# Kernel optimization log

Hardware: AMD Instinct MI355X
Metric: run time of the kernel (lower is better)

The kernel has to match this reference:

```python
import jax, jax.numpy as jnp
import numpy as np

N, NFEAT, NHID, K = 10000, 3000, 32, 10
ALPHA = 0.2


def setup_inputs() -> dict:
    key = jax.random.key(0)
    k1, k2, k3, k4, k5 = jax.random.split(key, 5)
    stdv = 1.0 / np.sqrt(NHID)
    x = jax.random.normal(k1, (N, NFEAT), dtype=jnp.float32)
    adj = jax.random.uniform(k2, (N, N), dtype=jnp.float32) / N  # row-stochastic-ish
    W = jax.random.uniform(k3, (NFEAT, NHID), minval=-stdv, maxval=stdv, dtype=jnp.float32)
    b = jax.random.uniform(k4, (NHID,), minval=-stdv, maxval=stdv, dtype=jnp.float32)
    mu = jax.random.normal(k5, (K, NHID), dtype=jnp.float32)
    return {"x": x, "adj": adj, "W": W, "b": b, "mu": mu}


def reference(x, adj, W, b, mu):
    # GCN layer: adj @ (x @ W) + b
    support = jnp.matmul(x, W)            # [N, NHID]
    z = jnp.matmul(adj, support) + b      # [N, NHID]
    # Student-t soft assignment (computed without materializing [N, K, NHID]):
    # ||z_i - mu_j||^2 = |z_i|^2 - 2 z_i.mu_j + |mu_j|^2
    z2 = jnp.sum(z * z, axis=1, keepdims=True)        # [N, 1]
    mu2 = jnp.sum(mu * mu, axis=1)                    # [K]
    d2 = z2 - 2.0 * jnp.matmul(z, mu.T) + mu2         # [N, K]
    q = 1.0 / (1.0 + d2 / ALPHA + 1e-08)
    q = q ** (ALPHA + 1.0) / 2.0
    q = q / jnp.sum(q, axis=1, keepdims=True)
    return z, q
```

## Files before the change

kernel.cpp:

```cpp
#include <hip/hip_runtime.h>
#include <math.h>


#define NH     32
#define KC     32
#define TR     256
#define LDA_S  36
#define NSPLIT 16

__global__ __launch_bounds__(256) void gemm_nt32(
    const float* __restrict__ A,
    const float* __restrict__ B,
    float* __restrict__ outp,
    int M, int K, int nchunks)
{
    __shared__ float As[TR * LDA_S];
    __shared__ float Bs[KC * NH];

    const int tid  = threadIdx.x;
    const int rg   = tid >> 2;
    const int jg   = tid & 3;
    const int row0 = blockIdx.x * TR;
    const int sy   = blockIdx.y;

    float acc[4][8];
#pragma unroll
    for (int m = 0; m < 4; ++m)
#pragma unroll
        for (int j = 0; j < 8; ++j) acc[m][j] = 0.0f;

    for (int c = sy; c < nchunks; c += NSPLIT) {
        const int k0 = c * KC;

#pragma unroll
        for (int p = 0; p < 8; ++p) {
            int idx = tid + (p << 8);
            int ar  = idx >> 3;
            int ac4 = idx & 7;
            int gr  = row0 + ar;
            int gk  = k0 + (ac4 << 2);
            float4 v = make_float4(0.f, 0.f, 0.f, 0.f);
            if (gr < M && gk < K)
                v = *(const float4*)(A + (size_t)gr * K + gk);
            *(float4*)(&As[ar * LDA_S + (ac4 << 2)]) = v;
        }
        {
            int brow = tid >> 3;
            int bc4  = tid & 7;
            int gk   = k0 + brow;
            float4 v = make_float4(0.f, 0.f, 0.f, 0.f);
            if (gk < K)
                v = *(const float4*)(B + (size_t)gk * NH + (bc4 << 2));
            *(float4*)(&Bs[brow * NH + (bc4 << 2)]) = v;
        }
        __syncthreads();

#pragma unroll
        for (int kk = 0; kk < KC; kk += 4) {
            float4 a[4];
#pragma unroll
            for (int m = 0; m < 4; ++m)
                a[m] = *(const float4*)(&As[(rg + (m << 6)) * LDA_S + kk]);
#pragma unroll
            for (int t = 0; t < 4; ++t) {
                float4 b0 = *(const float4*)(&Bs[(kk + t) * NH + (jg << 3)]);
                float4 b1 = *(const float4*)(&Bs[(kk + t) * NH + (jg << 3) + 4]);
#pragma unroll
                for (int m = 0; m < 4; ++m) {
                    float av = (t == 0) ? a[m].x : (t == 1) ? a[m].y
                             : (t == 2) ? a[m].z : a[m].w;
                    acc[m][0] += av * b0.x;
                    acc[m][1] += av * b0.y;
                    acc[m][2] += av * b0.z;
                    acc[m][3] += av * b0.w;
                    acc[m][4] += av * b1.x;
                    acc[m][5] += av * b1.y;
                    acc[m][6] += av * b1.z;
                    acc[m][7] += av * b1.w;
                }
            }
        }
        __syncthreads();
    }

    float* op = outp + (size_t)sy * M * NH;
#pragma unroll
    for (int m = 0; m < 4; ++m) {
        int gr = row0 + rg + (m << 6);
        if (gr < M) {
            float4 v0 = make_float4(acc[m][0], acc[m][1], acc[m][2], acc[m][3]);
            float4 v1 = make_float4(acc[m][4], acc[m][5], acc[m][6], acc[m][7]);
            *(float4*)(op + (size_t)gr * NH + (jg << 3))     = v0;
            *(float4*)(op + (size_t)gr * NH + (jg << 3) + 4) = v1;
        }
    }
}

__global__ __launch_bounds__(256) void reduce_add(
    const float* __restrict__ parts,
    const float* __restrict__ bias,
    float* __restrict__ out,
    int total4)
{
    int i = blockIdx.x * blockDim.x + threadIdx.x;
    if (i >= total4) return;
    float4 s = make_float4(0.f, 0.f, 0.f, 0.f);
#pragma unroll
    for (int p = 0; p < NSPLIT; ++p) {
        float4 v = ((const float4*)parts)[(size_t)p * total4 + i];
        s.x += v.x; s.y += v.y; s.z += v.z; s.w += v.w;
    }
    if (bias) {
        float4 bv = ((const float4*)bias)[i & 7];
        s.x += bv.x; s.y += bv.y; s.z += bv.z; s.w += bv.w;
    }
    ((float4*)out)[i] = s;
}

__global__ __launch_bounds__(256) void qkern(
    const float* __restrict__ z,
    const float* __restrict__ mu,
    float* __restrict__ q,
    int N)
{
    const int tid  = threadIdx.x;
    const int lane = tid & 31;
    const int i    = blockIdx.x * 8 + (tid >> 5);
    if (i >= N) return;

    float zv = z[i * 32 + lane];
    float qm = 0.f, qsum = 0.f;
#pragma unroll
    for (int c = 0; c < 10; ++c) {
        float d = zv - mu[c * 32 + lane];
        float p = d * d;
#pragma unroll
        for (int m = 16; m >= 1; m >>= 1) p += __shfl_xor(p, m, 32);
        float t  = 1.0f + p * 5.0f + 1e-8f;
        float qc = powf(t, -1.2f) * 0.5f;
        qsum += qc;
        if (lane == c) qm = qc;
    }
    if (lane < 10) q[i * 10 + lane] = qm / qsum;
}

extern "C" void kernel_launch(void* const* d_in, const int* in_sizes, int n_in,
                              void* d_out, int out_size, void* d_ws, size_t ws_size,
                              hipStream_t stream)
{
    const float* x   = (const float*)d_in[0];
    const float* adj = (const float*)d_in[1];
    const float* W   = (const float*)d_in[2];
    const float* b   = (const float*)d_in[3];
    const float* mu  = (const float*)d_in[4];

    const int N = 10000, NFEAT = 3000;
    float* z_out = (float*)d_out;
    float* q_out = (float*)d_out + N * NH;

    float* ws_part    = (float*)d_ws;
    float* ws_support = (float*)d_ws + (size_t)NSPLIT * N * NH;

    const int total4   = N * NH / 4;
    const int rowBlks  = (N + TR - 1) / TR;
    const int redBlks  = (total4 + 255) / 256;

    {
        int nchunks = (NFEAT + KC - 1) / KC;
        gemm_nt32<<<dim3(rowBlks, NSPLIT), 256, 0, stream>>>(
            x, W, ws_part, N, NFEAT, nchunks);
    }
    reduce_add<<<redBlks, 256, 0, stream>>>(ws_part, nullptr, ws_support, total4);
    {
        int nchunks = (N + KC - 1) / KC;
        gemm_nt32<<<dim3(rowBlks, NSPLIT), 256, 0, stream>>>(
            adj, ws_support, ws_part, N, N, nchunks);
    }
    reduce_add<<<redBlks, 256, 0, stream>>>(ws_part, b, z_out, total4);
    qkern<<<(N + 7) / 8, 256, 0, stream>>>(z_out, mu, q_out, N);
}
```

Measured before the change: 835.5 us.

## Stream A rows directly from global with register double-buffering, contiguous K splits

The skinny GEMM no longer stages the A tile in shared memory. Each thread reads its four rows straight from global memory as float4s, prefetching the next 8-wide chunk into registers while computing the current one. Each block now covers one contiguous K range and loads large 320-row B slabs into LDS, and the split count doubles to 32 when the workspace allows. This removes the LDS round-trip and the per-32-K syncs on the bandwidth-bound adj read, at the cost of uncoalesced per-thread strided global loads and larger partial-sum reductions.

```diff
diff --git a/kernel.cpp b/kernel.cpp
--- a/kernel.cpp
+++ b/kernel.cpp
@@ -2,26 +2,62 @@
 #include <math.h>
 
 
-#define NH     32
-#define KC     32
-#define TR     256
-#define LDA_S  36
-#define NSPLIT 16
-
-__global__ __launch_bounds__(256) void gemm_nt32(
+#define NH   32
+#define SUBK 320
+#define TRB  256
+
+__device__ __forceinline__ void fma8x4(const float4* __restrict__ bs, int jg2,
+                                       const float4* a0, const float4* a1,
+                                       float acc[4][8])
+{
+#pragma unroll
+    for (int u = 0; u < 2; ++u) {
+#pragma unroll
+        for (int t = 0; t < 4; ++t) {
+            float4 b0 = bs[(u * 4 + t) * 8 + jg2];
+            float4 b1 = bs[(u * 4 + t) * 8 + jg2 + 1];
+#pragma unroll
+            for (int m = 0; m < 4; ++m) {
+                float4 am = u ? a1[m] : a0[m];
+                float av = (t == 0) ? am.x : (t == 1) ? am.y
+                         : (t == 2) ? am.z : am.w;
+                acc[m][0] += av * b0.x;
+                acc[m][1] += av * b0.y;
+                acc[m][2] += av * b0.z;
+                acc[m][3] += av * b0.w;
+                acc[m][4] += av * b1.x;
+                acc[m][5] += av * b1.y;
+                acc[m][6] += av * b1.z;
+                acc[m][7] += av * b1.w;
+            }
+        }
+    }
+}
+
+__global__ __launch_bounds__(256) void gemm_stream32(
     const float* __restrict__ A,
     const float* __restrict__ B,
     float* __restrict__ outp,
-    int M, int K, int nchunks)
-{
-    __shared__ float As[TR * LDA_S];
-    __shared__ float Bs[KC * NH];
-
-    const int tid  = threadIdx.x;
-    const int rg   = tid >> 2;
-    const int jg   = tid & 3;
-    const int row0 = blockIdx.x * TR;
-    const int sy   = blockIdx.y;
+    int M, int K, int CH)
+{
+    __shared__ float Bs[SUBK * NH];
+
+    const int tid     = threadIdx.x;
+    const int rowslot = tid >> 2;
+    const int jg      = tid & 3;
+    const int jg2     = jg << 1;
+    const int row0    = blockIdx.x * TRB;
+    const int sy      = blockIdx.y;
+    const int k0      = sy * CH;
+    const int kspl    = min(CH, K - k0);
+
+    const float* ap[4];
+#pragma unroll
+    for (int m = 0; m < 4; ++m) {
+        int r = row0 + rowslot + (m << 6);
+        if (r > M - 1) r = M - 1;
+        ap[m] = A + (size_t)r * K + k0;
+    }
 
     float acc[4][8];
 #pragma unroll
@@ -29,56 +65,42 @@
 #pragma unroll
         for (int j = 0; j < 8; ++j) acc[m][j] = 0.0f;
 
-    for (int c = sy; c < nchunks; c += NSPLIT) {
-        const int k0 = c * KC;
-
-#pragma unroll
-        for (int p = 0; p < 8; ++p) {
-            int idx = tid + (p << 8);
-            int ar  = idx >> 3;
-            int ac4 = idx & 7;
-            int gr  = row0 + ar;
-            int gk  = k0 + (ac4 << 2);
-            float4 v = make_float4(0.f, 0.f, 0.f, 0.f);
-            if (gr < M && gk < K)
-                v = *(const float4*)(A + (size_t)gr * K + gk);
-            *(float4*)(&As[ar * LDA_S + (ac4 << 2)]) = v;
-        }
+    for (int kb = 0; kb < kspl; kb += SUBK) {
+        const int kcnt = min(SUBK, kspl - kb);
+
         {
-            int brow = tid >> 3;
-            int bc4  = tid & 7;
-            int gk   = k0 + brow;
-            float4 v = make_float4(0.f, 0.f, 0.f, 0.f);
-            if (gk < K)
-                v = *(const float4*)(B + (size_t)gk * NH + (bc4 << 2));
-            *(float4*)(&Bs[brow * NH + (bc4 << 2)]) = v;
+            const float4* src = (const float4*)(B + (size_t)(k0 + kb) * NH);
+            float4* dst = (float4*)Bs;
+            for (int i = tid; i < kcnt * 8; i += 256) dst[i] = src[i];
         }
         __syncthreads();
 
-#pragma unroll
-        for (int kk = 0; kk < KC; kk += 4) {
-            float4 a[4];
-#pragma unroll
-            for (int m = 0; m < 4; ++m)
-                a[m] = *(const float4*)(&As[(rg + (m << 6)) * LDA_S + kk]);
-#pragma unroll
-            for (int t = 0; t < 4; ++t) {
-                float4 b0 = *(const float4*)(&Bs[(kk + t) * NH + (jg << 3)]);
-                float4 b1 = *(const float4*)(&Bs[(kk + t) * NH + (jg << 3) + 4]);
+        float4 A0[4], A1[4], B0[4], B1[4];
+#pragma unroll
+        for (int m = 0; m < 4; ++m) {
+            A0[m] = *(const float4*)(ap[m] + kb);
+            A1[m] = *(const float4*)(ap[m] + kb + 4);
+        }
+
+        int kk = 0;
+        for (; kk + 16 <= kcnt; kk += 16) {
+#pragma unroll
+            for (int m = 0; m < 4; ++m) {
+                B0[m] = *(const float4*)(ap[m] + kb + kk + 8);
+                B1[m] = *(const float4*)(ap[m] + kb + kk + 12);
+            }
+            fma8x4(((const float4*)Bs) + kk * 8, jg2, A0, A1, acc);
+            if (kk + 16 < kcnt) {
 #pragma unroll
                 for (int m = 0; m < 4; ++m) {
-                    float av = (t == 0) ? a[m].x : (t == 1) ? a[m].y
-                             : (t == 2) ? a[m].z : a[m].w;
-                    acc[m][0] += av * b0.x;
-                    acc[m][1] += av * b0.y;
-                    acc[m][2] += av * b0.z;
-                    acc[m][3] += av * b0.w;
-                    acc[m][4] += av * b1.x;
-                    acc[m][5] += av * b1.y;
-                    acc[m][6] += av * b1.z;
-                    acc[m][7] += av * b1.w;
+                    A0[m] = *(const float4*)(ap[m] + kb + kk + 16);
+                    A1[m] = *(const float4*)(ap[m] + kb + kk + 20);
                 }
             }
+            fma8x4(((const float4*)Bs) + (kk + 8) * 8, jg2, B0, B1, acc);
+        }
+        if (kk < kcnt) {
+            fma8x4(((const float4*)Bs) + kk * 8, jg2, A0, A1, acc);
         }
         __syncthreads();
     }
@@ -86,7 +108,7 @@
     float* op = outp + (size_t)sy * M * NH;
 #pragma unroll
     for (int m = 0; m < 4; ++m) {
-        int gr = row0 + rg + (m << 6);
+        int gr = row0 + rowslot + (m << 6);
         if (gr < M) {
             float4 v0 = make_float4(acc[m][0], acc[m][1], acc[m][2], acc[m][3]);
             float4 v1 = make_float4(acc[m][4], acc[m][5], acc[m][6], acc[m][7]);
@@ -100,13 +122,12 @@
     const float* __restrict__ parts,
     const float* __restrict__ bias,
     float* __restrict__ out,
-    int total4)
+    int total4, int nsplit)
 {
     int i = blockIdx.x * blockDim.x + threadIdx.x;
     if (i >= total4) return;
     float4 s = make_float4(0.f, 0.f, 0.f, 0.f);
-#pragma unroll
-    for (int p = 0; p < NSPLIT; ++p) {
+    for (int p = 0; p < nsplit; ++p) {
         float4 v = ((const float4*)parts)[(size_t)p * total4 + i];
         s.x += v.x; s.y += v.y; s.z += v.z; s.w += v.w;
     }
@@ -158,24 +179,24 @@
     float* z_out = (float*)d_out;
     float* q_out = (float*)d_out + N * NH;
 
+    const size_t need32 = (size_t)(32 + 1) * N * NH * sizeof(float);
+    const int nsplit = (ws_size >= need32) ? 32 : 16;
+
     float* ws_part    = (float*)d_ws;
-    float* ws_support = (float*)d_ws + (size_t)NSPLIT * N * NH;
-
-    const int total4   = N * NH / 4;
-    const int rowBlks  = (N + TR - 1) / TR;
-    const int redBlks  = (total4 + 255) / 256;
-
-    {
-        int nchunks = (NFEAT + KC - 1) / KC;
-        gemm_nt32<<<dim3(rowBlks, NSPLIT), 256, 0, stream>>>(
-            x, W, ws_part, N, NFEAT, nchunks);
-    }
-    reduce_add<<<redBlks, 256, 0, stream>>>(ws_part, nullptr, ws_support, total4);
-    {
-        int nchunks = (N + KC - 1) / KC;
-        gemm_nt32<<<dim3(rowBlks, NSPLIT), 256, 0, stream>>>(
-            adj, ws_support, ws_part, N, N, nchunks);
-    }
-    reduce_add<<<redBlks, 256, 0, stream>>>(ws_part, b, z_out, total4);
+    float* ws_support = (float*)d_ws + (size_t)nsplit * N * NH;
+
+    const int total4  = N * NH / 4;
+    const int rowBlks = (N + TRB - 1) / TRB;
+    const int redBlks = (total4 + 255) / 256;
+
+    const int ch1 = ((NFEAT + nsplit - 1) / nsplit + 7) & ~7;
+    const int ch2 = ((N     + nsplit - 1) / nsplit + 7) & ~7;
+
+    gemm_stream32<<<dim3(rowBlks, nsplit), 256, 0, stream>>>(
+        x, W, ws_part, N, NFEAT, ch1);
+    reduce_add<<<redBlks, 256, 0, stream>>>(ws_part, nullptr, ws_support, total4, nsplit);
+    gemm_stream32<<<dim3(rowBlks, nsplit), 256, 0, stream>>>(
+        adj, ws_support, ws_part, N, N, ch2);
+    reduce_add<<<redBlks, 256, 0, stream>>>(ws_part, b, z_out, total4, nsplit);
     qkern<<<(N + 7) / 8, 256, 0, stream>>>(z_out, mu, q_out, N);
 }
```

Result: faster. 812.6 us (-2.7%).
